# Kernel tuning notes

Measured on AMD Instinct MI355X. Metric: run time of the kernel, lower is better.

The kernel has to match this reference:

```python
import jax, jax.numpy as jnp
from jax import lax
import numpy as np

B, C, H, W = 32, 1, 224, 224
F, KS = 64, 7

def setup_inputs() -> dict:
    key = jax.random.key(0)
    k1, k2 = jax.random.split(key)
    x = jax.random.normal(k1, (B, C, H, W), dtype=jnp.float32)
    # torch.rand -> uniform [0,1)
    kernel = jax.random.uniform(k2, (F, KS, KS), dtype=jnp.float32)
    return {"input": x, "kernel": kernel}

def reference(input, kernel):
    # Original: zero-pad by k//2 on all sides, then for each output pixel
    # out[b, f, i, j] = sum(patch[b, 0] * kernel[f]) -> single-input-channel conv.
    ks = kernel.shape[-1]
    pad = ks // 2
    w = kernel[:, None, :, :]  # [F, 1, ks, ks] in OIHW
    out = lax.conv_general_dilated(
        input, w,
        window_strides=(1, 1),
        padding=[(pad, pad), (pad, pad)],
        dimension_numbers=("NCHW", "OIHW", "NCHW"),
    )
    return out  # [B, F, H, W]
```

## Files before the change

kernel.cpp:

```cpp
#include <hip/hip_runtime.h>
#include <stdint.h>


#define H_     224
#define W_     224
#define B_     32
#define F_     64
#define KS_    7
#define TILE   32
#define LROWS  40
#define LPITCH 40
#define HW_    (H_ * W_)

typedef _Float16 f16x8 __attribute__((ext_vector_type(8)));
typedef float    f32x4 __attribute__((ext_vector_type(4)));

__global__ __launch_bounds__(256)
void Conv_58394375356438_kernel(const float* __restrict__ in,
                                const float* __restrict__ wt,
                                float* __restrict__ out)
{
    __shared__ uint32_t P[LROWS * LPITCH];

    const int blk = blockIdx.x;
    const int tx  = blk % (W_ / TILE);
    const int ty  = (blk / (W_ / TILE)) % (H_ / TILE);
    const int b   = blk / ((W_ / TILE) * (H_ / TILE));
    const int x0  = tx * TILE;
    const int y0  = ty * TILE;

    const float* __restrict__ inp = in + (size_t)b * HW_;

    for (int i = threadIdx.x; i < LROWS * LPITCH; i += 256) {
        const int rr = i / LPITCH;
        const int jj = i - rr * LPITCH;
        const int gy = y0 - 3 + rr;
        const int gx = x0 - 3 + jj;
        float v0 = 0.0f, v1 = 0.0f;
        if (gy >= 0 && gy < H_) {
            const float* row = inp + gy * W_;
            if (gx >= 0 && gx < W_)         v0 = row[gx];
            if (gx + 1 >= 0 && gx + 1 < W_) v1 = row[gx + 1];
        }
        union { _Float16 h[2]; uint32_t u; } pk;
        pk.h[0] = (_Float16)v0;
        pk.h[1] = (_Float16)v1;
        P[i] = pk.u;
    }

    const int lane = threadIdx.x & 63;
    const int g    = lane >> 4;
    const int fr   = lane & 15;

    f16x8 afr[4][2];
    #pragma unroll
    for (int t = 0; t < 4; ++t) {
        #pragma unroll
        for (int kf = 0; kf < 2; ++kf) {
            const int ky = kf * 4 + g;
            const float* wrow = wt + (t * 16 + fr) * (KS_ * KS_) + ky * KS_;
            f16x8 a;
            #pragma unroll
            for (int kx = 0; kx < 8; ++kx) {
                const float w = (ky < KS_ && kx < KS_) ? wrow[kx] : 0.0f;
                a[kx] = (_Float16)w;
            }
            afr[t][kf] = a;
        }
    }

    __syncthreads();

    const int wave = threadIdx.x >> 6;
    const int p    = lane & 15;

    float* __restrict__ outbase =
        out + ((size_t)(b * F_ + 4 * g) * H_ + y0) * W_ + x0 + p;

    for (int rr = 0; rr < 8; ++rr) {
        const int r = wave * 8 + rr;
        #pragma unroll
        for (int xb = 0; xb < TILE; xb += 16) {
            const int base0 = (r + g) * LPITCH + xb + p;

            union { f16x8 v; uint32_t u[4]; } b0, b1;
            b0.u[0] = P[base0 + 0];
            b0.u[1] = P[base0 + 2];
            b0.u[2] = P[base0 + 4];
            b0.u[3] = P[base0 + 6];
            b1.u[0] = P[base0 + 4 * LPITCH + 0];
            b1.u[1] = P[base0 + 4 * LPITCH + 2];
            b1.u[2] = P[base0 + 4 * LPITCH + 4];
            b1.u[3] = P[base0 + 4 * LPITCH + 6];

            f32x4 acc[4];
            #pragma unroll
            for (int t = 0; t < 4; ++t) acc[t] = (f32x4){0.f, 0.f, 0.f, 0.f};

            #pragma unroll
            for (int t = 0; t < 4; ++t) {
                acc[t] = __builtin_amdgcn_mfma_f32_16x16x32_f16(afr[t][0], b0.v, acc[t], 0, 0, 0);
                acc[t] = __builtin_amdgcn_mfma_f32_16x16x32_f16(afr[t][1], b1.v, acc[t], 0, 0, 0);
            }

            #pragma unroll
            for (int t = 0; t < 4; ++t) {
                #pragma unroll
                for (int j = 0; j < 4; ++j) {
                    outbase[(size_t)(t * 16 + j) * HW_ + r * W_ + xb] = acc[t][j];
                }
            }
        }
    }
}

extern "C" void kernel_launch(void* const* d_in, const int* in_sizes, int n_in,
                              void* d_out, int out_size, void* d_ws, size_t ws_size,
                              hipStream_t stream)
{
    const float* in = (const float*)d_in[0];
    const float* wt = (const float*)d_in[1];
    float* out      = (float*)d_out;

    const int grid = B_ * (H_ / TILE) * (W_ / TILE);
    Conv_58394375356438_kernel<<<grid, 256, 0, stream>>>(in, wt, out);
}
```

Before: 435.9 us.

## Swap MFMA operands so outputs store as 16-byte vectors along width

Each block now covers 4 full-width output rows instead of a 32x32 tile, and each wave handles one row across all 224 columns. The MFMA operands are swapped (pixels as A, weights as B) so each lane holds 4 consecutive x positions for a single filter, which allows one 16-byte vector store per filter group instead of scattered scalar stores. The output write is the dominant cost, so this aims for more coalesced writes. The shared tile is wider and carries a larger halo ratio in rows (11 staged rows for 4 output rows).

```diff
diff --git a/kernel.cpp b/kernel.cpp
--- a/kernel.cpp
+++ b/kernel.cpp
@@ -2,57 +2,56 @@
 #include <stdint.h>
 
 
-#define H_     224
-#define W_     224
-#define B_     32
-#define F_     64
-#define KS_    7
-#define TILE   32
-#define LROWS  40
-#define LPITCH 40
-#define HW_    (H_ * W_)
+#define H_    224
+#define W_    224
+#define B_    32
+#define F_    64
+#define KS_   7
+#define ROWS  4
+#define LROWS (ROWS + 7)
+#define PITCH 232
+#define HW_   (H_ * W_)
 
 typedef _Float16 f16x8 __attribute__((ext_vector_type(8)));
 typedef float    f32x4 __attribute__((ext_vector_type(4)));
+typedef uint32_t u32x4 __attribute__((ext_vector_type(4)));
 
 __global__ __launch_bounds__(256)
 void Conv_58394375356438_kernel(const float* __restrict__ in,
                                 const float* __restrict__ wt,
                                 float* __restrict__ out)
 {
-    __shared__ uint32_t P[LROWS * LPITCH];
+    __shared__ uint32_t P[LROWS * PITCH];
 
     const int blk = blockIdx.x;
-    const int tx  = blk % (W_ / TILE);
-    const int ty  = (blk / (W_ / TILE)) % (H_ / TILE);
-    const int b   = blk / ((W_ / TILE) * (H_ / TILE));
-    const int x0  = tx * TILE;
-    const int y0  = ty * TILE;
+    const int yb  = blk % (H_ / ROWS);
+    const int b   = blk / (H_ / ROWS);
+    const int y0  = yb * ROWS;
 
     const float* __restrict__ inp = in + (size_t)b * HW_;
 
-    for (int i = threadIdx.x; i < LROWS * LPITCH; i += 256) {
-        const int rr = i / LPITCH;
-        const int jj = i - rr * LPITCH;
-        const int gy = y0 - 3 + rr;
-        const int gx = x0 - 3 + jj;
+    for (int idx = threadIdx.x; idx < LROWS * PITCH; idx += 256) {
+        const int lr = idx / PITCH;
+        const int i  = idx - lr * PITCH;
+        const int gy = y0 - 3 + lr;
+        const int gx = i - 3;
         float v0 = 0.0f, v1 = 0.0f;
         if (gy >= 0 && gy < H_) {
-            const float* row = inp + gy * W_;
-            if (gx >= 0 && gx < W_)         v0 = row[gx];
-            if (gx + 1 >= 0 && gx + 1 < W_) v1 = row[gx + 1];
+            const float* __restrict__ row = inp + gy * W_;
+            if (gx >= 0 && gx < W_)        v0 = row[gx];
+            if (gx >= -1 && gx + 1 < W_)   v1 = row[gx + 1];
         }
         union { _Float16 h[2]; uint32_t u; } pk;
         pk.h[0] = (_Float16)v0;
         pk.h[1] = (_Float16)v1;
-        P[i] = pk.u;
+        P[idx] = pk.u;
     }
 
     const int lane = threadIdx.x & 63;
     const int g    = lane >> 4;
     const int fr   = lane & 15;
 
-    f16x8 afr[4][2];
+    f16x8 wfr[4][2];
     #pragma unroll
     for (int t = 0; t < 4; ++t) {
         #pragma unroll
@@ -65,52 +64,50 @@
                 const float w = (ky < KS_ && kx < KS_) ? wrow[kx] : 0.0f;
                 a[kx] = (_Float16)w;
             }
-            afr[t][kf] = a;
+            wfr[t][kf] = a;
         }
     }
 
     __syncthreads();
 
     const int wave = threadIdx.x >> 6;
-    const int p    = lane & 15;
+    const int y    = y0 + wave;
 
-    float* __restrict__ outbase =
-        out + ((size_t)(b * F_ + 4 * g) * H_ + y0) * W_ + x0 + p;
+    const uint32_t* __restrict__ p0 = &P[(wave + g) * PITCH];
+    const uint32_t* __restrict__ p1 = &P[(wave + g + 4) * PITCH];
 
-    for (int rr = 0; rr < 8; ++rr) {
-        const int r = wave * 8 + rr;
-        #pragma unroll
-        for (int xb = 0; xb < TILE; xb += 16) {
-            const int base0 = (r + g) * LPITCH + xb + p;
+    float* __restrict__ ob0 = out + ((size_t)(b * F_ +  0 + fr) * H_ + y) * W_ + 4 * g;
+    float* __restrict__ ob1 = out + ((size_t)(b * F_ + 16 + fr) * H_ + y) * W_ + 4 * g;
+    float* __restrict__ ob2 = out + ((size_t)(b * F_ + 32 + fr) * H_ + y) * W_ + 4 * g;
+    float* __restrict__ ob3 = out + ((size_t)(b * F_ + 48 + fr) * H_ + y) * W_ + 4 * g;
 
-            union { f16x8 v; uint32_t u[4]; } b0, b1;
-            b0.u[0] = P[base0 + 0];
-            b0.u[1] = P[base0 + 2];
-            b0.u[2] = P[base0 + 4];
-            b0.u[3] = P[base0 + 6];
-            b1.u[0] = P[base0 + 4 * LPITCH + 0];
-            b1.u[1] = P[base0 + 4 * LPITCH + 2];
-            b1.u[2] = P[base0 + 4 * LPITCH + 4];
-            b1.u[3] = P[base0 + 4 * LPITCH + 6];
+    #pragma unroll
+    for (int xg = 0; xg < W_ / 16; ++xg) {
+        const int i0 = xg * 16 + fr;
+        u32x4 q0, q1;
+        q0[0] = p0[i0];     q0[1] = p0[i0 + 2];
+        q0[2] = p0[i0 + 4]; q0[3] = p0[i0 + 6];
+        q1[0] = p1[i0];     q1[1] = p1[i0 + 2];
+        q1[2] = p1[i0 + 4]; q1[3] = p1[i0 + 6];
+        const f16x8 pf0 = __builtin_bit_cast(f16x8, q0);
+        const f16x8 pf1 = __builtin_bit_cast(f16x8, q1);
 
-            f32x4 acc[4];
-            #pragma unroll
-            for (int t = 0; t < 4; ++t) acc[t] = (f32x4){0.f, 0.f, 0.f, 0.f};
+        f32x4 a0 = {0.f, 0.f, 0.f, 0.f};
+        f32x4 a1 = a0, a2 = a0, a3 = a0;
 
-            #pragma unroll
-            for (int t = 0; t < 4; ++t) {
-                acc[t] = __builtin_amdgcn_mfma_f32_16x16x32_f16(afr[t][0], b0.v, acc[t], 0, 0, 0);
-                acc[t] = __builtin_amdgcn_mfma_f32_16x16x32_f16(afr[t][1], b1.v, acc[t], 0, 0, 0);
-            }
+        a0 = __builtin_amdgcn_mfma_f32_16x16x32_f16(pf0, wfr[0][0], a0, 0, 0, 0);
+        a1 = __builtin_amdgcn_mfma_f32_16x16x32_f16(pf0, wfr[1][0], a1, 0, 0, 0);
+        a2 = __builtin_amdgcn_mfma_f32_16x16x32_f16(pf0, wfr[2][0], a2, 0, 0, 0);
+        a3 = __builtin_amdgcn_mfma_f32_16x16x32_f16(pf0, wfr[3][0], a3, 0, 0, 0);
+        a0 = __builtin_amdgcn_mfma_f32_16x16x32_f16(pf1, wfr[0][1], a0, 0, 0, 0);
+        a1 = __builtin_amdgcn_mfma_f32_16x16x32_f16(pf1, wfr[1][1], a1, 0, 0, 0);
+        a2 = __builtin_amdgcn_mfma_f32_16x16x32_f16(pf1, wfr[2][1], a2, 0, 0, 0);
+        a3 = __builtin_amdgcn_mfma_f32_16x16x32_f16(pf1, wfr[3][1], a3, 0, 0, 0);
 
-            #pragma unroll
-            for (int t = 0; t < 4; ++t) {
-                #pragma unroll
-                for (int j = 0; j < 4; ++j) {
-                    outbase[(size_t)(t * 16 + j) * HW_ + r * W_ + xb] = acc[t][j];
-                }
-            }
-        }
+        *reinterpret_cast<f32x4*>(ob0 + xg * 16) = a0;
+        *reinterpret_cast<f32x4*>(ob1 + xg * 16) = a1;
+        *reinterpret_cast<f32x4*>(ob2 + xg * 16) = a2;
+        *reinterpret_cast<f32x4*>(ob3 + xg * 16) = a3;
     }
 }
 
@@ -122,6 +119,6 @@
     const float* wt = (const float*)d_in[1];
     float* out      = (float*)d_out;
 
-    const int grid = B_ * (H_ / TILE) * (W_ / TILE);
+    const int grid = B_ * (H_ / ROWS);
     Conv_58394375356438_kernel<<<grid, 256, 0, stream>>>(in, wt, out);
 }
```

After: 434.6 us. No clear change (-0.3%).
